# Optimization experiments

Measured on AMD Instinct MI355X. Metric: run time of the kernel, lower is better.

Reference implementation:

```python
import jax, jax.numpy as jnp
import numpy as np

N_NODES = 59392        # batch_size * node_each_graph = 512 * 116
N_EDGES = 1187840      # avg degree 20

def _graph_conv(h, src, dst, W, b, out_norm, in_norm):
    # DGL GraphConv, norm='both': act((D_in^-1/2 A D_out^-1/2 h) W + b)
    h = h * out_norm[:, None]
    m = jax.ops.segment_sum(h[src], dst, num_segments=N_NODES)  # sparse aggregation
    m = m * in_norm[:, None]
    return jax.nn.relu(m @ W + b)

def setup_inputs() -> dict:
    key = jax.random.key(0)
    ks = jax.random.split(key, 8)
    feat = jax.random.normal(ks[0], (N_NODES, 116), dtype=jnp.float32)
    src = jax.random.randint(ks[1], (N_EDGES,), 0, N_NODES)
    dst = jax.random.randint(ks[2], (N_EDGES,), 0, N_NODES)
    W1 = jax.random.normal(ks[3], (116, 64), dtype=jnp.float32) * 0.05
    b1 = jnp.zeros((64,), dtype=jnp.float32)
    W2 = jax.random.normal(ks[4], (64, 64), dtype=jnp.float32) * 0.05
    b2 = jnp.zeros((64,), dtype=jnp.float32)
    Wc = jax.random.normal(ks[5], (116 * 64, 2), dtype=jnp.float32) * 0.05
    bc = jnp.zeros((2,), dtype=jnp.float32)
    return {"feat": feat, "src": src, "dst": dst, "batch_size": 512,
            "W1": W1, "b1": b1, "W2": W2, "b2": b2, "Wc": Wc, "bc": bc}

def reference(feat, src, dst, batch_size, W1, b1, W2, b2, Wc, bc):
    ones = jnp.ones((N_EDGES,), dtype=jnp.float32)
    out_deg = jax.ops.segment_sum(ones, src, num_segments=N_NODES)
    in_deg = jax.ops.segment_sum(ones, dst, num_segments=N_NODES)
    out_norm = jax.lax.rsqrt(jnp.maximum(out_deg, 1.0))
    in_norm = jax.lax.rsqrt(jnp.maximum(in_deg, 1.0))
    h = _graph_conv(feat, src, dst, W1, b1, out_norm, in_norm)
    # dropout is identity in eval mode
    h = _graph_conv(h, src, dst, W2, b2, out_norm, in_norm)
    h = h.reshape(batch_size, -1)  # (B, node_each_graph * hid)
    return h @ Wc + bc
```

## Files before the change

### kernel.cpp

```cpp
#include <hip/hip_runtime.h>

#define N_NODES 59392
#define N_EDGES 1187840
#define F_IN 116
#define F_HID 64
#define BATCH 512
#define NPG 116
#define CCAP 64
#define NSLD 160
#define EPSD (N_EDGES / NSLD)
#define NSLS 64
#define EPSS (N_EDGES / NSLS)
#define NR 4
#define NPR4 (N_NODES / NR)
#define GPB 4
#define NPB (NPG / GPB)
#define SCAN_BLK (N_NODES / 256)
#define GEMM_BLK 640

typedef __attribute__((ext_vector_type(8))) short short8;
typedef __attribute__((ext_vector_type(4))) float float4v;

__device__ __forceinline__ float u2f(unsigned u) {
    union { unsigned u; float f; } x; x.u = u; return x.f;
}
__device__ __forceinline__ float bf2f(unsigned short h) {
    union { unsigned u; float f; } x; x.u = (unsigned)h << 16; return x.f;
}
__device__ __forceinline__ unsigned short f2bf(float f) {
    union { float f; unsigned u; } x; x.f = f;
    unsigned r = x.u + 0x7FFF + ((x.u >> 16) & 1);
    return (unsigned short)(r >> 16);
}

__global__ __launch_bounds__(256) void hist_kernel(const int* __restrict__ src,
                                                   const int* __restrict__ dst,
                                                   unsigned short* __restrict__ cnt2,
                                                   unsigned short* __restrict__ cnt2s) {
    __shared__ unsigned bins[NPR4 / 2];
    int tid = threadIdx.x;
    int b = blockIdx.x;
    const int* __restrict__ idx;
    unsigned short* outp;
    int slice, range, nedge;
    if (b < NSLD * NR) {
        slice = b >> 2; range = b & 3; idx = dst; outp = cnt2; nedge = EPSD;
    } else {
        int bb = b - NSLD * NR;
        slice = bb >> 2; range = bb & 3; idx = src; outp = cnt2s; nedge = EPSS;
    }
    int r0 = range * NPR4;
    long ebase = (long)slice * nedge;
    for (int k = tid; k < NPR4 / 2; k += 256) bins[k] = 0;
    __syncthreads();
    for (int k = tid; k < nedge; k += 256) {
        int v = idx[ebase + k] - r0;
        if ((unsigned)v < NPR4) atomicAdd(&bins[v >> 1], 1u << ((v & 1) * 16));
    }
    __syncthreads();
    unsigned* op = (unsigned*)(outp + (size_t)slice * N_NODES + r0);
    for (int k = tid; k < NPR4 / 2; k += 256) op[k] = bins[k];
}

__global__ __launch_bounds__(256) void scan_gemm1_kernel(unsigned short* __restrict__ cnt2,
                                                         const unsigned short* __restrict__ cnt2s,
                                                         float* __restrict__ onorm,
                                                         float* __restrict__ inorm,
                                                         int* __restrict__ ncnt,
                                                         const float* __restrict__ feat,
                                                         const float* __restrict__ W1,
                                                         unsigned short* __restrict__ A1h) {
    if (blockIdx.x < SCAN_BLK) {
        int d = blockIdx.x * 256 + threadIdx.x;
        int run = 0;
        #pragma unroll 1
        for (int i = 0; i < NSLD; i += 8) {
            int c[8];
            #pragma unroll
            for (int j = 0; j < 8; ++j) c[j] = cnt2[(size_t)(i + j) * N_NODES + d];
            #pragma unroll
            for (int j = 0; j < 8; ++j) {
                cnt2[(size_t)(i + j) * N_NODES + d] = (unsigned short)run;
                run += c[j];
            }
        }
        int o = 0;
        #pragma unroll 1
        for (int i = 0; i < NSLS; i += 8) {
            int c[8];
            #pragma unroll
            for (int j = 0; j < 8; ++j) c[j] = cnt2s[(size_t)(i + j) * N_NODES + d];
            #pragma unroll
            for (int j = 0; j < 8; ++j) o += c[j];
        }
        onorm[d] = rsqrtf(fmaxf((float)o, 1.0f));
        inorm[d] = rsqrtf(fmaxf((float)run, 1.0f));
        ncnt[d] = run < CCAP ? run : CCAP;
        if (d == 0) onorm[N_NODES] = 0.f;
        return;
    }
    int lane = threadIdx.x & 63;
    int c16 = lane & 15, quad = lane >> 4;
    short8 Bhi[4][4], Blo[4][4];
    #pragma unroll
    for (int kiter = 0; kiter < 4; ++kiter) {
        #pragma unroll
        for (int t = 0; t < 4; ++t) {
            #pragma unroll
            for (int j = 0; j < 8; ++j) {
                int k = kiter * 32 + quad * 8 + j;
                float w = (k < F_IN) ? W1[k * F_HID + t * 16 + c16] : 0.f;
                unsigned short hi = f2bf(w);
                unsigned short lo = f2bf(w - bf2f(hi));
                Bhi[kiter][t][j] = (short)hi;
                Blo[kiter][t][j] = (short)lo;
            }
        }
    }
    int bid = blockIdx.x - SCAN_BLK;
    int wid = (bid * 256 + threadIdx.x) >> 6;
    int nwaves = (GEMM_BLK * 256) >> 6;
    const int ntiles = N_NODES / 16;
    for (int tile = wid; tile < ntiles; tile += nwaves) {
        int base = tile * 16;
        int row = base + c16;
        const float* fp = feat + (size_t)row * F_IN;
        float4v acc[4] = {{0.f,0.f,0.f,0.f},{0.f,0.f,0.f,0.f},{0.f,0.f,0.f,0.f},{0.f,0.f,0.f,0.f}};
        #pragma unroll
        for (int kiter = 0; kiter < 4; ++kiter) {
            int koff = kiter * 32 + quad * 8;
            float f[8];
            if (koff + 8 <= F_IN) {
                float4 x = *(const float4*)(fp + koff);
                float4 y = *(const float4*)(fp + koff + 4);
                f[0]=x.x; f[1]=x.y; f[2]=x.z; f[3]=x.w;
                f[4]=y.x; f[5]=y.y; f[6]=y.z; f[7]=y.w;
            } else {
                #pragma unroll
                for (int j = 0; j < 8; ++j) f[j] = (koff + j < F_IN) ? fp[koff + j] : 0.f;
            }
            short8 ah, al;
            #pragma unroll
            for (int j = 0; j < 8; ++j) {
                float v = f[j];
                unsigned short hi = f2bf(v);
                ah[j] = (short)hi;
                al[j] = (short)f2bf(v - bf2f(hi));
            }
            #pragma unroll
            for (int t = 0; t < 4; ++t) {
                acc[t] = __builtin_amdgcn_mfma_f32_16x16x32_bf16(ah, Bhi[kiter][t], acc[t], 0, 0, 0);
                acc[t] = __builtin_amdgcn_mfma_f32_16x16x32_bf16(al, Bhi[kiter][t], acc[t], 0, 0, 0);
                acc[t] = __builtin_amdgcn_mfma_f32_16x16x32_bf16(ah, Blo[kiter][t], acc[t], 0, 0, 0);
            }
        }
        #pragma unroll
        for (int t = 0; t < 4; ++t) {
            #pragma unroll
            for (int r = 0; r < 4; ++r) {
                int node = base + quad * 4 + r;
                A1h[(size_t)node * F_HID + t * 16 + c16] = f2bf(acc[t][r]);
            }
        }
    }
}

__global__ __launch_bounds__(256) void place_kernel(const int* __restrict__ src,
                                                    const int* __restrict__ dst,
                                                    const unsigned short* __restrict__ cnt2,
                                                    unsigned short* __restrict__ ebuf) {
    __shared__ unsigned cur[NPR4 / 2];
    int tid = threadIdx.x;
    int slice = blockIdx.x >> 2;
    int r0 = (blockIdx.x & 3) * NPR4;
    long ebase = (long)slice * EPSD;
    const unsigned* pp = (const unsigned*)(cnt2 + (size_t)slice * N_NODES + r0);
    for (int k = tid; k < NPR4 / 2; k += 256) cur[k] = pp[k];
    __syncthreads();
    #pragma unroll 1
    for (int t = 0; t < 7; ++t) {
        int k = t * 1024 + tid;
        int d0 = dst[ebase + k],        s0 = src[ebase + k];
        int d1 = dst[ebase + k + 256],  s1 = src[ebase + k + 256];
        int d2 = dst[ebase + k + 512],  s2 = src[ebase + k + 512];
        int d3 = dst[ebase + k + 768],  s3 = src[ebase + k + 768];
        #define PLACE1(dd, ss)                                                    \
            { int dr = (dd) - r0;                                                 \
              if ((unsigned)dr < NPR4) {                                          \
                  int sh = (dr & 1) * 16;                                         \
                  unsigned old = atomicAdd(&cur[dr >> 1], 1u << sh);              \
                  unsigned pos = (old >> sh) & 0xFFFFu;                           \
                  if (pos < CCAP) ebuf[(size_t)(dd) * CCAP + pos] = (unsigned short)(ss); } }
        PLACE1(d0, s0) PLACE1(d1, s1) PLACE1(d2, s2) PLACE1(d3, s3)
    }
    {
        int k = 7168 + tid;
        int d0 = dst[ebase + k], s0 = src[ebase + k];
        PLACE1(d0, s0)
        #undef PLACE1
    }
}

template<bool ON>
__device__ __forceinline__ void gather2n(const unsigned* __restrict__ base,
                                         const unsigned short* __restrict__ ebuf,
                                         const float* __restrict__ onorm,
                                         int va, int vb, int na, int nb,
                                         int c16, int g4, int sh16,
                                         float& a0, float& a1, float& a2, float& a3,
                                         float& b0, float& b1, float& b2, float& b3) {
    const unsigned long long* ea = (const unsigned long long*)(ebuf + (size_t)va * CCAP);
    const unsigned long long* eb = (const unsigned long long*)(ebuf + (size_t)vb * CCAP);
    unsigned long long cha[8], chb[8];
    #pragma unroll
    for (int t = 0; t < 8; ++t) cha[t] = ea[t];
    #pragma unroll
    for (int t = 0; t < 8; ++t) chb[t] = eb[t];
    int ida[8], idb[8];
    #pragma unroll
    for (int t = 0; t < 8; ++t) {
        ida[t] = (t * 4 + g4 < na) ? (int)((cha[t] >> sh16) & 0xFFFFu) : N_NODES;
        idb[t] = (t * 4 + g4 < nb) ? (int)((chb[t] >> sh16) & 0xFFFFu) : N_NODES;
    }
    unsigned long long rwa[8], rwb[8];
    #pragma unroll
    for (int t = 0; t < 8; ++t) rwa[t] = *(const unsigned long long*)(base + ida[t] * 32 + c16 * 2);
    #pragma unroll
    for (int t = 0; t < 8; ++t) rwb[t] = *(const unsigned long long*)(base + idb[t] * 32 + c16 * 2);
    float oa[8], ob[8];
    if constexpr (ON) {
        #pragma unroll
        for (int t = 0; t < 8; ++t) { oa[t] = onorm[ida[t]]; ob[t] = onorm[idb[t]]; }
    }
    #pragma unroll
    for (int t = 0; t < 8; ++t) {
        unsigned lo = (unsigned)rwa[t], hi = (unsigned)(rwa[t] >> 32);
        float s = ON ? oa[t] : 1.f;
        a0 += s * u2f(lo << 16); a1 += s * u2f(lo & 0xFFFF0000u);
        a2 += s * u2f(hi << 16); a3 += s * u2f(hi & 0xFFFF0000u);
    }
    #pragma unroll
    for (int t = 0; t < 8; ++t) {
        unsigned lo = (unsigned)rwb[t], hi = (unsigned)(rwb[t] >> 32);
        float s = ON ? ob[t] : 1.f;
        b0 += s * u2f(lo << 16); b1 += s * u2f(lo & 0xFFFF0000u);
        b2 += s * u2f(hi << 16); b3 += s * u2f(hi & 0xFFFF0000u);
    }
    int nqa = (na + 3) >> 2;
    #pragma unroll 1
    for (int t = 8; t < nqa; ++t) {
        unsigned long long c = ea[t];
        int e = t * 4 + g4;
        int ix = (e < na) ? (int)((c >> sh16) & 0xFFFFu) : N_NODES;
        unsigned long long w = *(const unsigned long long*)(base + ix * 32 + c16 * 2);
        unsigned lo = (unsigned)w, hi = (unsigned)(w >> 32);
        float s = 1.f;
        if constexpr (ON) s = onorm[ix];
        a0 += s * u2f(lo << 16); a1 += s * u2f(lo & 0xFFFF0000u);
        a2 += s * u2f(hi << 16); a3 += s * u2f(hi & 0xFFFF0000u);
    }
    int nqb = (nb + 3) >> 2;
    #pragma unroll 1
    for (int t = 8; t < nqb; ++t) {
        unsigned long long c = eb[t];
        int e = t * 4 + g4;
        int ix = (e < nb) ? (int)((c >> sh16) & 0xFFFFu) : N_NODES;
        unsigned long long w = *(const unsigned long long*)(base + ix * 32 + c16 * 2);
        unsigned lo = (unsigned)w, hi = (unsigned)(w >> 32);
        float s = 1.f;
        if constexpr (ON) s = onorm[ix];
        b0 += s * u2f(lo << 16); b1 += s * u2f(lo & 0xFFFF0000u);
        b2 += s * u2f(hi << 16); b3 += s * u2f(hi & 0xFFFF0000u);
    }
    a0 += __shfl_xor(a0, 16); a1 += __shfl_xor(a1, 16);
    a2 += __shfl_xor(a2, 16); a3 += __shfl_xor(a3, 16);
    a0 += __shfl_xor(a0, 32); a1 += __shfl_xor(a1, 32);
    a2 += __shfl_xor(a2, 32); a3 += __shfl_xor(a3, 32);
    b0 += __shfl_xor(b0, 16); b1 += __shfl_xor(b1, 16);
    b2 += __shfl_xor(b2, 16); b3 += __shfl_xor(b3, 16);
    b0 += __shfl_xor(b0, 32); b1 += __shfl_xor(b1, 32);
    b2 += __shfl_xor(b2, 32); b3 += __shfl_xor(b3, 32);
}

__global__ __launch_bounds__(256) void gather1_kernel(const int* __restrict__ ncnt,
                                                      const unsigned short* __restrict__ ebuf,
                                                      const unsigned short* __restrict__ A1h,
                                                      const float* __restrict__ onorm,
                                                      const float* __restrict__ inorm,
                                                      const float* __restrict__ b1,
                                                      unsigned short* __restrict__ H1h,
                                                      float* __restrict__ out) {
    if (blockIdx.x == 0) {
        int t = threadIdx.x;
        for (int k = t; k < BATCH * 2; k += 256) out[k] = 0.f;
        if (t < 16) ((unsigned long long*)(H1h + (size_t)N_NODES * F_HID))[t] = 0ull;
    }
    int lane = threadIdx.x & 63;
    int wu = __builtin_amdgcn_readfirstlane(threadIdx.x >> 6);
    int c16 = lane & 15, g4 = lane >> 4, sh16 = g4 * 16;
    int va = blockIdx.x * 8 + wu * 2;
    int vb = va + 1;
    int na = ncnt[va], nb = ncnt[vb];
    const unsigned* base = (const unsigned*)A1h;
    float4 b1q = ((const float4*)b1)[c16];
    float a0 = 0.f, a1 = 0.f, a2 = 0.f, a3 = 0.f;
    float b0 = 0.f, b1v = 0.f, b2v = 0.f, b3 = 0.f;
    gather2n<true>(base, ebuf, onorm, va, vb, na, nb, c16, g4, sh16,
                   a0, a1, a2, a3, b0, b1v, b2v, b3);
    float ina = inorm[va], ona = onorm[va];
    float inb = inorm[vb], onb = onorm[vb];
    float ha0 = fmaxf(ina * a0 + b1q.x, 0.f) * ona;
    float ha1 = fmaxf(ina * a1 + b1q.y, 0.f) * ona;
    float ha2 = fmaxf(ina * a2 + b1q.z, 0.f) * ona;
    float ha3 = fmaxf(ina * a3 + b1q.w, 0.f) * ona;
    float hb0 = fmaxf(inb * b0 + b1q.x, 0.f) * onb;
    float hb1 = fmaxf(inb * b1v + b1q.y, 0.f) * onb;
    float hb2 = fmaxf(inb * b2v + b1q.z, 0.f) * onb;
    float hb3 = fmaxf(inb * b3 + b1q.w, 0.f) * onb;
    if (g4 == 0) {
        unsigned lo = (unsigned)f2bf(ha0) | ((unsigned)f2bf(ha1) << 16);
        unsigned hi = (unsigned)f2bf(ha2) | ((unsigned)f2bf(ha3) << 16);
        ((unsigned long long*)H1h)[(size_t)va * 16 + c16] = ((unsigned long long)hi << 32) | lo;
        lo = (unsigned)f2bf(hb0) | ((unsigned)f2bf(hb1) << 16);
        hi = (unsigned)f2bf(hb2) | ((unsigned)f2bf(hb3) << 16);
        ((unsigned long long*)H1h)[(size_t)vb * 16 + c16] = ((unsigned long long)hi << 32) | lo;
    }
}

__global__ __launch_bounds__(256) void readout_kernel(const int* __restrict__ ncnt,
                                                      const unsigned short* __restrict__ ebuf,
                                                      const unsigned short* __restrict__ H1h,
                                                      const float* __restrict__ inorm,
                                                      const float* __restrict__ b2,
                                                      const float* __restrict__ W2,
                                                      const float* __restrict__ Wc,
                                                      const float* __restrict__ bc,
                                                      float* __restrict__ out) {
    __shared__ float Gs[NPB][F_HID];
    __shared__ float ls[8];
    int g = blockIdx.x >> 2, part = blockIdx.x & 3;
    int nbase = g * NPG + part * NPB;
    int lane = threadIdx.x & 63;
    int wu = __builtin_amdgcn_readfirstlane(threadIdx.x >> 6);
    int c16 = lane & 15, g4 = lane >> 4, sh16 = g4 * 16;
    const unsigned* base = (const unsigned*)H1h;
    for (int nl = wu * 2; nl + 1 < NPB; nl += 8) {
        int va = nbase + nl, vb = va + 1;
        int na = ncnt[va], nb = ncnt[vb];
        float a0 = 0.f, a1 = 0.f, a2 = 0.f, a3 = 0.f;
        float b0 = 0.f, b1 = 0.f, b2v = 0.f, b3 = 0.f;
        gather2n<false>(base, ebuf, (const float*)nullptr, va, vb, na, nb, c16, g4, sh16,
                        a0, a1, a2, a3, b0, b1, b2v, b3);
        if (g4 == 0) {
            float4 m4; m4.x = a0; m4.y = a1; m4.z = a2; m4.w = a3;
            *(float4*)&Gs[nl][c16 * 4] = m4;
            m4.x = b0; m4.y = b1; m4.z = b2v; m4.w = b3;
            *(float4*)&Gs[nl + 1][c16 * 4] = m4;
        }
    }
    if (wu == 2) {
        int v = nbase + 28;
        int n = ncnt[v];
        float a0 = 0.f, a1 = 0.f, a2 = 0.f, a3 = 0.f;
        float d0 = 0.f, d1 = 0.f, d2 = 0.f, d3 = 0.f;
        gather2n<false>(base, ebuf, (const float*)nullptr, v, v, n, 0, c16, g4, sh16,
                        a0, a1, a2, a3, d0, d1, d2, d3);
        if (g4 == 0) {
            float4 m4; m4.x = a0; m4.y = a1; m4.z = a2; m4.w = a3;
            *(float4*)&Gs[28][c16 * 4] = m4;
        }
    }
    __syncthreads();
    float w2[F_HID];
    #pragma unroll
    for (int k = 0; k < F_HID; ++k) w2[k] = W2[k * F_HID + lane];
    float b2l = b2[lane];
    float s0 = 0.f, s1 = 0.f;
    for (int nl = wu; nl < NPB; nl += 4) {
        int v = nbase + nl;
        float acc = 0.f;
        #pragma unroll
        for (int k = 0; k < F_HID; k += 4) {
            float4 gk = *(const float4*)&Gs[nl][k];
            acc += gk.x * w2[k] + gk.y * w2[k + 1] + gk.z * w2[k + 2] + gk.w * w2[k + 3];
        }
        float h = fmaxf(inorm[v] * acc + b2l, 0.f);
        float2 w = ((const float2*)Wc)[(part * NPB + nl) * F_HID + lane];
        s0 += h * w.x;
        s1 += h * w.y;
    }
    #pragma unroll
    for (int off = 32; off > 0; off >>= 1) {
        s0 += __shfl_down(s0, off);
        s1 += __shfl_down(s1, off);
    }
    if (lane == 0) { ls[wu * 2] = s0; ls[wu * 2 + 1] = s1; }
    __syncthreads();
    if (threadIdx.x < 2) {
        float t = 0.f;
        #pragma unroll
        for (int w = 0; w < 4; ++w) t += ls[w * 2 + threadIdx.x];
        if (part == 0) t += bc[threadIdx.x];
        atomicAdd(&out[g * 2 + threadIdx.x], t);
    }
}

extern "C" void kernel_launch(void* const* d_in, const int* in_sizes, int n_in,
                              void* d_out, int out_size, void* d_ws, size_t ws_size,
                              hipStream_t stream) {
    const float* feat = (const float*)d_in[0];
    const int*   src  = (const int*)d_in[1];
    const int*   dst  = (const int*)d_in[2];
    const float* W1 = (const float*)d_in[4];
    const float* b1 = (const float*)d_in[5];
    const float* W2 = (const float*)d_in[6];
    const float* b2 = (const float*)d_in[7];
    const float* Wc = (const float*)d_in[8];
    const float* bc = (const float*)d_in[9];
    float* out = (float*)d_out;

    unsigned short* cnt2  = (unsigned short*)d_ws;
    unsigned short* cnt2s = cnt2 + (size_t)NSLD * N_NODES;
    float* onorm = (float*)(cnt2s + (size_t)NSLS * N_NODES);
    float* inorm = onorm + N_NODES + 1;
    int* ncnt    = (int*)(inorm + N_NODES);
    unsigned short* ebuf = (unsigned short*)(ncnt + N_NODES);
    unsigned short* A1h  = ebuf + (size_t)N_NODES * CCAP;
    unsigned short* H1h  = cnt2;

    hist_kernel<<<NSLD * NR + NSLS * NR, 256, 0, stream>>>(src, dst, cnt2, cnt2s);
    scan_gemm1_kernel<<<SCAN_BLK + GEMM_BLK, 256, 0, stream>>>(cnt2, cnt2s, onorm, inorm,
                                                               ncnt, feat, W1, A1h);
    place_kernel<<<NSLD * NR, 256, 0, stream>>>(src, dst, cnt2, ebuf);
    gather1_kernel<<<N_NODES / 8, 256, 0, stream>>>(ncnt, ebuf, A1h, onorm, inorm, b1, H1h, out);
    readout_kernel<<<BATCH * GPB, 256, 0, stream>>>(ncnt, ebuf, H1h, inorm, b2, W2, Wc, bc, out);
}
```

Baseline: 225.2 us.

## Split hidden features into two 32-wide halves for gathers with nontemporal loads

Stores the layer-1 projected features and hidden activations as two separate 32-feature bf16 arrays instead of one 64-feature array. Both gather kernels now make two passes, one per half, with 8 lanes covering a row and 8 edges handled in parallel per wavefront. The aim is to shrink the working set per pass so the randomly gathered rows stay in cache, and to spread edge parallelism wider across lanes. Edge-list reads and hidden-state writes become nontemporal. The cost is reading the edge list twice and running an extra shuffle reduction step.

```diff
diff --git a/kernel.cpp b/kernel.cpp
--- a/kernel.cpp
+++ b/kernel.cpp
@@ -69,7 +69,8 @@
                                                          int* __restrict__ ncnt,
                                                          const float* __restrict__ feat,
                                                          const float* __restrict__ W1,
-                                                         unsigned short* __restrict__ A1h) {
+                                                         unsigned short* __restrict__ A1lo,
+                                                         unsigned short* __restrict__ A1hi) {
     if (blockIdx.x < SCAN_BLK) {
         int d = blockIdx.x * 256 + threadIdx.x;
         int run = 0;
@@ -156,10 +157,12 @@
         }
         #pragma unroll
         for (int t = 0; t < 4; ++t) {
+            unsigned short* outp = (t < 2) ? A1lo : A1hi;
+            int fo = (t & 1) * 16 + c16;
             #pragma unroll
             for (int r = 0; r < 4; ++r) {
                 int node = base + quad * 4 + r;
-                A1h[(size_t)node * F_HID + t * 16 + c16] = f2bf(acc[t][r]);
+                outp[(size_t)node * 32 + fo] = f2bf(acc[t][r]);
             }
         }
     }
@@ -202,134 +205,140 @@
 }
 
 template<bool ON>
-__device__ __forceinline__ void gather2n(const unsigned* __restrict__ base,
-                                         const unsigned short* __restrict__ ebuf,
-                                         const float* __restrict__ onorm,
-                                         int va, int vb, int na, int nb,
-                                         int c16, int g4, int sh16,
-                                         float& a0, float& a1, float& a2, float& a3,
-                                         float& b0, float& b1, float& b2, float& b3) {
+__device__ __forceinline__ void gath2(const unsigned* __restrict__ base,
+                                      const unsigned short* __restrict__ ebuf,
+                                      const float* __restrict__ onorm,
+                                      int va, int vb, int na, int nb,
+                                      int c8, int g8,
+                                      float* __restrict__ A, float* __restrict__ B) {
     const unsigned long long* ea = (const unsigned long long*)(ebuf + (size_t)va * CCAP);
     const unsigned long long* eb = (const unsigned long long*)(ebuf + (size_t)vb * CCAP);
-    unsigned long long cha[8], chb[8];
-    #pragma unroll
-    for (int t = 0; t < 8; ++t) cha[t] = ea[t];
-    #pragma unroll
-    for (int t = 0; t < 8; ++t) chb[t] = eb[t];
-    int ida[8], idb[8];
-    #pragma unroll
-    for (int t = 0; t < 8; ++t) {
-        ida[t] = (t * 4 + g4 < na) ? (int)((cha[t] >> sh16) & 0xFFFFu) : N_NODES;
-        idb[t] = (t * 4 + g4 < nb) ? (int)((chb[t] >> sh16) & 0xFFFFu) : N_NODES;
-    }
-    unsigned long long rwa[8], rwb[8];
-    #pragma unroll
-    for (int t = 0; t < 8; ++t) rwa[t] = *(const unsigned long long*)(base + ida[t] * 32 + c16 * 2);
-    #pragma unroll
-    for (int t = 0; t < 8; ++t) rwb[t] = *(const unsigned long long*)(base + idb[t] * 32 + c16 * 2);
-    float oa[8], ob[8];
+    int qi = g8 >> 2;
+    int sh = (g8 & 3) * 16;
+    unsigned long long cha[4], chb[4];
+    #pragma unroll
+    for (int t = 0; t < 4; ++t) {
+        cha[t] = __builtin_nontemporal_load(&ea[2 * t + qi]);
+        chb[t] = __builtin_nontemporal_load(&eb[2 * t + qi]);
+    }
+    int ida[4], idb[4];
+    #pragma unroll
+    for (int t = 0; t < 4; ++t) {
+        ida[t] = (t * 8 + g8 < na) ? (int)((cha[t] >> sh) & 0xFFFFu) : N_NODES;
+        idb[t] = (t * 8 + g8 < nb) ? (int)((chb[t] >> sh) & 0xFFFFu) : N_NODES;
+    }
+    unsigned long long rwa[4], rwb[4];
+    #pragma unroll
+    for (int t = 0; t < 4; ++t) rwa[t] = *(const unsigned long long*)(base + ida[t] * 16 + c8 * 2);
+    #pragma unroll
+    for (int t = 0; t < 4; ++t) rwb[t] = *(const unsigned long long*)(base + idb[t] * 16 + c8 * 2);
+    float oa[4], ob[4];
     if constexpr (ON) {
         #pragma unroll
-        for (int t = 0; t < 8; ++t) { oa[t] = onorm[ida[t]]; ob[t] = onorm[idb[t]]; }
-    }
-    #pragma unroll
-    for (int t = 0; t < 8; ++t) {
+        for (int t = 0; t < 4; ++t) { oa[t] = onorm[ida[t]]; ob[t] = onorm[idb[t]]; }
+    }
+    #pragma unroll
+    for (int t = 0; t < 4; ++t) {
         unsigned lo = (unsigned)rwa[t], hi = (unsigned)(rwa[t] >> 32);
         float s = ON ? oa[t] : 1.f;
-        a0 += s * u2f(lo << 16); a1 += s * u2f(lo & 0xFFFF0000u);
-        a2 += s * u2f(hi << 16); a3 += s * u2f(hi & 0xFFFF0000u);
-    }
-    #pragma unroll
-    for (int t = 0; t < 8; ++t) {
+        A[0] += s * u2f(lo << 16); A[1] += s * u2f(lo & 0xFFFF0000u);
+        A[2] += s * u2f(hi << 16); A[3] += s * u2f(hi & 0xFFFF0000u);
+    }
+    #pragma unroll
+    for (int t = 0; t < 4; ++t) {
         unsigned lo = (unsigned)rwb[t], hi = (unsigned)(rwb[t] >> 32);
         float s = ON ? ob[t] : 1.f;
-        b0 += s * u2f(lo << 16); b1 += s * u2f(lo & 0xFFFF0000u);
-        b2 += s * u2f(hi << 16); b3 += s * u2f(hi & 0xFFFF0000u);
-    }
-    int nqa = (na + 3) >> 2;
+        B[0] += s * u2f(lo << 16); B[1] += s * u2f(lo & 0xFFFF0000u);
+        B[2] += s * u2f(hi << 16); B[3] += s * u2f(hi & 0xFFFF0000u);
+    }
+    int nqa = (na + 7) >> 3;
     #pragma unroll 1
-    for (int t = 8; t < nqa; ++t) {
-        unsigned long long c = ea[t];
-        int e = t * 4 + g4;
-        int ix = (e < na) ? (int)((c >> sh16) & 0xFFFFu) : N_NODES;
-        unsigned long long w = *(const unsigned long long*)(base + ix * 32 + c16 * 2);
+    for (int t = 4; t < nqa; ++t) {
+        unsigned long long c = __builtin_nontemporal_load(&ea[2 * t + qi]);
+        int ix = (t * 8 + g8 < na) ? (int)((c >> sh) & 0xFFFFu) : N_NODES;
+        unsigned long long w = *(const unsigned long long*)(base + ix * 16 + c8 * 2);
         unsigned lo = (unsigned)w, hi = (unsigned)(w >> 32);
         float s = 1.f;
         if constexpr (ON) s = onorm[ix];
-        a0 += s * u2f(lo << 16); a1 += s * u2f(lo & 0xFFFF0000u);
-        a2 += s * u2f(hi << 16); a3 += s * u2f(hi & 0xFFFF0000u);
-    }
-    int nqb = (nb + 3) >> 2;
+        A[0] += s * u2f(lo << 16); A[1] += s * u2f(lo & 0xFFFF0000u);
+        A[2] += s * u2f(hi << 16); A[3] += s * u2f(hi & 0xFFFF0000u);
+    }
+    int nqb = (nb + 7) >> 3;
     #pragma unroll 1
-    for (int t = 8; t < nqb; ++t) {
-        unsigned long long c = eb[t];
-        int e = t * 4 + g4;
-        int ix = (e < nb) ? (int)((c >> sh16) & 0xFFFFu) : N_NODES;
-        unsigned long long w = *(const unsigned long long*)(base + ix * 32 + c16 * 2);
+    for (int t = 4; t < nqb; ++t) {
+        unsigned long long c = __builtin_nontemporal_load(&eb[2 * t + qi]);
+        int ix = (t * 8 + g8 < nb) ? (int)((c >> sh) & 0xFFFFu) : N_NODES;
+        unsigned long long w = *(const unsigned long long*)(base + ix * 16 + c8 * 2);
         unsigned lo = (unsigned)w, hi = (unsigned)(w >> 32);
         float s = 1.f;
         if constexpr (ON) s = onorm[ix];
-        b0 += s * u2f(lo << 16); b1 += s * u2f(lo & 0xFFFF0000u);
-        b2 += s * u2f(hi << 16); b3 += s * u2f(hi & 0xFFFF0000u);
-    }
-    a0 += __shfl_xor(a0, 16); a1 += __shfl_xor(a1, 16);
-    a2 += __shfl_xor(a2, 16); a3 += __shfl_xor(a3, 16);
-    a0 += __shfl_xor(a0, 32); a1 += __shfl_xor(a1, 32);
-    a2 += __shfl_xor(a2, 32); a3 += __shfl_xor(a3, 32);
-    b0 += __shfl_xor(b0, 16); b1 += __shfl_xor(b1, 16);
-    b2 += __shfl_xor(b2, 16); b3 += __shfl_xor(b3, 16);
-    b0 += __shfl_xor(b0, 32); b1 += __shfl_xor(b1, 32);
-    b2 += __shfl_xor(b2, 32); b3 += __shfl_xor(b3, 32);
+        B[0] += s * u2f(lo << 16); B[1] += s * u2f(lo & 0xFFFF0000u);
+        B[2] += s * u2f(hi << 16); B[3] += s * u2f(hi & 0xFFFF0000u);
+    }
+    #pragma unroll
+    for (int j = 0; j < 4; ++j) {
+        A[j] += __shfl_xor(A[j], 8);  B[j] += __shfl_xor(B[j], 8);
+        A[j] += __shfl_xor(A[j], 16); B[j] += __shfl_xor(B[j], 16);
+        A[j] += __shfl_xor(A[j], 32); B[j] += __shfl_xor(B[j], 32);
+    }
 }
 
 __global__ __launch_bounds__(256) void gather1_kernel(const int* __restrict__ ncnt,
                                                       const unsigned short* __restrict__ ebuf,
-                                                      const unsigned short* __restrict__ A1h,
+                                                      const unsigned short* __restrict__ A1lo,
+                                                      const unsigned short* __restrict__ A1hi,
                                                       const float* __restrict__ onorm,
                                                       const float* __restrict__ inorm,
                                                       const float* __restrict__ b1,
-                                                      unsigned short* __restrict__ H1h,
+                                                      unsigned short* __restrict__ H1lo,
+                                                      unsigned short* __restrict__ H1hi,
                                                       float* __restrict__ out) {
     if (blockIdx.x == 0) {
         int t = threadIdx.x;
         for (int k = t; k < BATCH * 2; k += 256) out[k] = 0.f;
-        if (t < 16) ((unsigned long long*)(H1h + (size_t)N_NODES * F_HID))[t] = 0ull;
+        if (t < 8) ((unsigned long long*)(H1lo + (size_t)N_NODES * 32))[t] = 0ull;
+        else if (t < 16) ((unsigned long long*)(H1hi + (size_t)N_NODES * 32))[t - 8] = 0ull;
     }
     int lane = threadIdx.x & 63;
     int wu = __builtin_amdgcn_readfirstlane(threadIdx.x >> 6);
-    int c16 = lane & 15, g4 = lane >> 4, sh16 = g4 * 16;
+    int c8 = lane & 7, g8 = lane >> 3;
     int va = blockIdx.x * 8 + wu * 2;
     int vb = va + 1;
     int na = ncnt[va], nb = ncnt[vb];
-    const unsigned* base = (const unsigned*)A1h;
-    float4 b1q = ((const float4*)b1)[c16];
-    float a0 = 0.f, a1 = 0.f, a2 = 0.f, a3 = 0.f;
-    float b0 = 0.f, b1v = 0.f, b2v = 0.f, b3 = 0.f;
-    gather2n<true>(base, ebuf, onorm, va, vb, na, nb, c16, g4, sh16,
-                   a0, a1, a2, a3, b0, b1v, b2v, b3);
     float ina = inorm[va], ona = onorm[va];
     float inb = inorm[vb], onb = onorm[vb];
-    float ha0 = fmaxf(ina * a0 + b1q.x, 0.f) * ona;
-    float ha1 = fmaxf(ina * a1 + b1q.y, 0.f) * ona;
-    float ha2 = fmaxf(ina * a2 + b1q.z, 0.f) * ona;
-    float ha3 = fmaxf(ina * a3 + b1q.w, 0.f) * ona;
-    float hb0 = fmaxf(inb * b0 + b1q.x, 0.f) * onb;
-    float hb1 = fmaxf(inb * b1v + b1q.y, 0.f) * onb;
-    float hb2 = fmaxf(inb * b2v + b1q.z, 0.f) * onb;
-    float hb3 = fmaxf(inb * b3 + b1q.w, 0.f) * onb;
-    if (g4 == 0) {
-        unsigned lo = (unsigned)f2bf(ha0) | ((unsigned)f2bf(ha1) << 16);
-        unsigned hi = (unsigned)f2bf(ha2) | ((unsigned)f2bf(ha3) << 16);
-        ((unsigned long long*)H1h)[(size_t)va * 16 + c16] = ((unsigned long long)hi << 32) | lo;
-        lo = (unsigned)f2bf(hb0) | ((unsigned)f2bf(hb1) << 16);
-        hi = (unsigned)f2bf(hb2) | ((unsigned)f2bf(hb3) << 16);
-        ((unsigned long long*)H1h)[(size_t)vb * 16 + c16] = ((unsigned long long)hi << 32) | lo;
+    #pragma unroll
+    for (int half = 0; half < 2; ++half) {
+        const unsigned* base = (const unsigned*)(half ? A1hi : A1lo);
+        unsigned short* H = half ? H1hi : H1lo;
+        float4 b1q = ((const float4*)b1)[half * 8 + c8];
+        float A[4] = {0.f,0.f,0.f,0.f}, B[4] = {0.f,0.f,0.f,0.f};
+        gath2<true>(base, ebuf, onorm, va, vb, na, nb, c8, g8, A, B);
+        float ha0 = fmaxf(ina * A[0] + b1q.x, 0.f) * ona;
+        float ha1 = fmaxf(ina * A[1] + b1q.y, 0.f) * ona;
+        float ha2 = fmaxf(ina * A[2] + b1q.z, 0.f) * ona;
+        float ha3 = fmaxf(ina * A[3] + b1q.w, 0.f) * ona;
+        float hb0 = fmaxf(inb * B[0] + b1q.x, 0.f) * onb;
+        float hb1 = fmaxf(inb * B[1] + b1q.y, 0.f) * onb;
+        float hb2 = fmaxf(inb * B[2] + b1q.z, 0.f) * onb;
+        float hb3 = fmaxf(inb * B[3] + b1q.w, 0.f) * onb;
+        if (g8 == 0) {
+            unsigned lo = (unsigned)f2bf(ha0) | ((unsigned)f2bf(ha1) << 16);
+            unsigned hi = (unsigned)f2bf(ha2) | ((unsigned)f2bf(ha3) << 16);
+            __builtin_nontemporal_store(((unsigned long long)hi << 32) | lo,
+                                        (unsigned long long*)H + (size_t)va * 8 + c8);
+            lo = (unsigned)f2bf(hb0) | ((unsigned)f2bf(hb1) << 16);
+            hi = (unsigned)f2bf(hb2) | ((unsigned)f2bf(hb3) << 16);
+            __builtin_nontemporal_store(((unsigned long long)hi << 32) | lo,
+                                        (unsigned long long*)H + (size_t)vb * 8 + c8);
+        }
     }
 }
 
 __global__ __launch_bounds__(256) void readout_kernel(const int* __restrict__ ncnt,
                                                       const unsigned short* __restrict__ ebuf,
-                                                      const unsigned short* __restrict__ H1h,
+                                                      const unsigned short* __restrict__ H1lo,
+                                                      const unsigned short* __restrict__ H1hi,
                                                       const float* __restrict__ inorm,
                                                       const float* __restrict__ b2,
                                                       const float* __restrict__ W2,
@@ -342,32 +351,31 @@
     int nbase = g * NPG + part * NPB;
     int lane = threadIdx.x & 63;
     int wu = __builtin_amdgcn_readfirstlane(threadIdx.x >> 6);
-    int c16 = lane & 15, g4 = lane >> 4, sh16 = g4 * 16;
-    const unsigned* base = (const unsigned*)H1h;
-    for (int nl = wu * 2; nl + 1 < NPB; nl += 8) {
-        int va = nbase + nl, vb = va + 1;
-        int na = ncnt[va], nb = ncnt[vb];
-        float a0 = 0.f, a1 = 0.f, a2 = 0.f, a3 = 0.f;
-        float b0 = 0.f, b1 = 0.f, b2v = 0.f, b3 = 0.f;
-        gather2n<false>(base, ebuf, (const float*)nullptr, va, vb, na, nb, c16, g4, sh16,
-                        a0, a1, a2, a3, b0, b1, b2v, b3);
-        if (g4 == 0) {
-            float4 m4; m4.x = a0; m4.y = a1; m4.z = a2; m4.w = a3;
-            *(float4*)&Gs[nl][c16 * 4] = m4;
-            m4.x = b0; m4.y = b1; m4.z = b2v; m4.w = b3;
-            *(float4*)&Gs[nl + 1][c16 * 4] = m4;
-        }
-    }
-    if (wu == 2) {
-        int v = nbase + 28;
-        int n = ncnt[v];
-        float a0 = 0.f, a1 = 0.f, a2 = 0.f, a3 = 0.f;
-        float d0 = 0.f, d1 = 0.f, d2 = 0.f, d3 = 0.f;
-        gather2n<false>(base, ebuf, (const float*)nullptr, v, v, n, 0, c16, g4, sh16,
-                        a0, a1, a2, a3, d0, d1, d2, d3);
-        if (g4 == 0) {
-            float4 m4; m4.x = a0; m4.y = a1; m4.z = a2; m4.w = a3;
-            *(float4*)&Gs[28][c16 * 4] = m4;
+    int c8 = lane & 7, g8 = lane >> 3;
+    #pragma unroll
+    for (int half = 0; half < 2; ++half) {
+        const unsigned* base = (const unsigned*)(half ? H1hi : H1lo);
+        for (int nl = wu * 2; nl + 1 < NPB; nl += 8) {
+            int va = nbase + nl, vb = va + 1;
+            int na = ncnt[va], nb = ncnt[vb];
+            float A[4] = {0.f,0.f,0.f,0.f}, B[4] = {0.f,0.f,0.f,0.f};
+            gath2<false>(base, ebuf, (const float*)nullptr, va, vb, na, nb, c8, g8, A, B);
+            if (g8 == 0) {
+                float4 m4; m4.x = A[0]; m4.y = A[1]; m4.z = A[2]; m4.w = A[3];
+                *(float4*)&Gs[nl][half * 32 + c8 * 4] = m4;
+                m4.x = B[0]; m4.y = B[1]; m4.z = B[2]; m4.w = B[3];
+                *(float4*)&Gs[nl + 1][half * 32 + c8 * 4] = m4;
+            }
+        }
+        if (wu == 2) {
+            int v = nbase + 28;
+            int n = ncnt[v];
+            float A[4] = {0.f,0.f,0.f,0.f}, D[4] = {0.f,0.f,0.f,0.f};
+            gath2<false>(base, ebuf, (const float*)nullptr, v, v, n, 0, c8, g8, A, D);
+            if (g8 == 0) {
+                float4 m4; m4.x = A[0]; m4.y = A[1]; m4.z = A[2]; m4.w = A[3];
+                *(float4*)&Gs[28][half * 32 + c8 * 4] = m4;
+            }
         }
     }
     __syncthreads();
@@ -425,13 +433,17 @@
     float* inorm = onorm + N_NODES + 1;
     int* ncnt    = (int*)(inorm + N_NODES);
     unsigned short* ebuf = (unsigned short*)(ncnt + N_NODES);
-    unsigned short* A1h  = ebuf + (size_t)N_NODES * CCAP;
-    unsigned short* H1h  = cnt2;
+    unsigned short* A1lo = ebuf + (size_t)N_NODES * CCAP;
+    unsigned short* A1hi = A1lo + (size_t)(N_NODES + 1) * 32;
+    unsigned short* H1lo = cnt2;
+    unsigned short* H1hi = H1lo + (size_t)(N_NODES + 1) * 32;
 
     hist_kernel<<<NSLD * NR + NSLS * NR, 256, 0, stream>>>(src, dst, cnt2, cnt2s);
     scan_gemm1_kernel<<<SCAN_BLK + GEMM_BLK, 256, 0, stream>>>(cnt2, cnt2s, onorm, inorm,
-                                                               ncnt, feat, W1, A1h);
+                                                               ncnt, feat, W1, A1lo, A1hi);
     place_kernel<<<NSLD * NR, 256, 0, stream>>>(src, dst, cnt2, ebuf);
-    gather1_kernel<<<N_NODES / 8, 256, 0, stream>>>(ncnt, ebuf, A1h, onorm, inorm, b1, H1h, out);
-    readout_kernel<<<BATCH * GPB, 256, 0, stream>>>(ncnt, ebuf, H1h, inorm, b2, W2, Wc, bc, out);
-}
+    gather1_kernel<<<N_NODES / 8, 256, 0, stream>>>(ncnt, ebuf, A1lo, A1hi, onorm, inorm,
+                                                    b1, H1lo, H1hi, out);
+    readout_kernel<<<BATCH * GPB, 256, 0, stream>>>(ncnt, ebuf, H1lo, H1hi, inorm, b2,
+                                                    W2, Wc, bc, out);
+}
```

Result: slower. 256.6 us (+13.9%).
